# Kernel optimization log

Measured on AMD Instinct MI355X. Metric: run time of the kernel, lower is better.

Reference implementation:

```python
import jax, jax.numpy as jnp
import numpy as np

NUM_ITEMS = 100000
EMB_DIM = 146          # total output feature width
N_GENRES = 18          # fixed genre one-hot width
BATCH = 1048576


def setup_inputs() -> dict:
    key = jax.random.key(0)
    k1, k2, k3 = jax.random.split(key, 3)
    item_inputs = jax.random.randint(k1, (BATCH,), 0, NUM_ITEMS, dtype=jnp.int64)
    # learned embedding table, width = embedding_dim - 18
    item_embedding = jax.random.normal(k2, (NUM_ITEMS, EMB_DIM - N_GENRES), dtype=jnp.float32)
    # precomputed dense genre table: row i = one-hot genre vector for item i
    # (0/1 entries; items missing from the dict are all-zero rows)
    genre_table = (jax.random.uniform(k3, (NUM_ITEMS, N_GENRES)) < 0.15).astype(jnp.float32)
    return {"item_inputs": item_inputs, "item_embedding": item_embedding, "genre_table": genre_table}


def reference(item_inputs, item_embedding, genre_table):
    # fused double gather + concat: [B, 128] ++ [B, 18] -> [B, 146]
    item_embeds = item_embedding[item_inputs]   # embedding lookup
    item_genres = genre_table[item_inputs]      # vectorized replacement of python dict loop
    return jnp.concatenate([item_embeds, item_genres], axis=1)
```

## Files before the change

### kernel.cpp

```cpp
#include <hip/hip_runtime.h>


#define ROW_F2   73u
#define EMB_F2   64u
#define GENRE_F2 9u
#define TOTAL_F2 (1048576u * ROW_F2)

__global__ __launch_bounds__(256) void item_emb_gather_concat(
    const int* __restrict__ idx,
    const float2* __restrict__ emb,
    const float2* __restrict__ genre,
    float2* __restrict__ out)
{
    unsigned g = blockIdx.x * blockDim.x + threadIdx.x;
    if (g >= TOTAL_F2) return;

    unsigned row = g / ROW_F2;
    unsigned c2  = g - row * ROW_F2;

    int item = idx[row];

    float2 v;
    if (c2 < EMB_F2) {
        v = emb[(unsigned long long)item * EMB_F2 + c2];
    } else {
        v = genre[(unsigned long long)item * GENRE_F2 + (c2 - EMB_F2)];
    }
    out[g] = v;
}

extern "C" void kernel_launch(void* const* d_in, const int* in_sizes, int n_in,
                              void* d_out, int out_size, void* d_ws, size_t ws_size,
                              hipStream_t stream) {
    const int*    idx   = (const int*)d_in[0];
    const float2* emb   = (const float2*)d_in[1];
    const float2* genre = (const float2*)d_in[2];
    float2*       out   = (float2*)d_out;

    const unsigned block = 256;
    const unsigned grid  = (TOTAL_F2 + block - 1) / block;
    item_emb_gather_concat<<<grid, block, 0, stream>>>(idx, emb, genre, out);
}
```

Baseline: 785.6 us.

## Assign four rows per wavefront with vectorized index load and nontemporal stores

Replaces the one-thread-per-float2 mapping with one wavefront per four output rows. Each wave loads its four indices with a single int4 load, has each lane gather one float2 of each embedding row, and spreads the four genre slices across 36 lanes. Outputs are written with nontemporal stores. This removes the per-element division, repeated index loads and divergent branching, but relies on BATCH being a multiple of 16 and leaves some lanes idle during the genre gather.

Result: faster. 736.8 us (-6.2%).

```diff
diff --git a/kernel.cpp b/kernel.cpp
--- a/kernel.cpp
+++ b/kernel.cpp
@@ -1,43 +1,61 @@
 #include <hip/hip_runtime.h>
 
 
-#define ROW_F2   73u
-#define EMB_F2   64u
-#define GENRE_F2 9u
-#define TOTAL_F2 (1048576u * ROW_F2)
+#define BATCH     1048576u
+#define ROW_F2    73u
+#define EMB_F2    64u
+#define GENRE_F2  9u
+#define ROWS_PW   4u
+
+typedef float f32x2 __attribute__((ext_vector_type(2)));
 
 __global__ __launch_bounds__(256) void item_emb_gather_concat(
-    const int* __restrict__ idx,
-    const float2* __restrict__ emb,
-    const float2* __restrict__ genre,
-    float2* __restrict__ out)
+    const int*   __restrict__ idx,
+    const f32x2* __restrict__ emb,
+    const f32x2* __restrict__ genre,
+    f32x2*       __restrict__ out)
 {
-    unsigned g = blockIdx.x * blockDim.x + threadIdx.x;
-    if (g >= TOTAL_F2) return;
+    const unsigned lane = threadIdx.x & 63u;
 
-    unsigned row = g / ROW_F2;
-    unsigned c2  = g - row * ROW_F2;
+    unsigned wid_v = (blockIdx.x * 256u + threadIdx.x) >> 6;
+    const unsigned wid = (unsigned)__builtin_amdgcn_readfirstlane((int)wid_v);
+    const unsigned r0  = wid * ROWS_PW;
 
-    int item = idx[row];
+    const int4 it4 = *reinterpret_cast<const int4*>(idx + r0);
+    const unsigned i0 = (unsigned)it4.x;
+    const unsigned i1 = (unsigned)it4.y;
+    const unsigned i2 = (unsigned)it4.z;
+    const unsigned i3 = (unsigned)it4.w;
 
-    float2 v;
-    if (c2 < EMB_F2) {
-        v = emb[(unsigned long long)item * EMB_F2 + c2];
-    } else {
-        v = genre[(unsigned long long)item * GENRE_F2 + (c2 - EMB_F2)];
-    }
-    out[g] = v;
+    f32x2 e0 = emb[(size_t)i0 * EMB_F2 + lane];
+    f32x2 e1 = emb[(size_t)i1 * EMB_F2 + lane];
+    f32x2 e2 = emb[(size_t)i2 * EMB_F2 + lane];
+    f32x2 e3 = emb[(size_t)i3 * EMB_F2 + lane];
+
+    unsigned ri = lane / 9u;
+    unsigned c  = lane - ri * 9u;
+    unsigned item = ri < 2u ? (ri == 0u ? i0 : i1)
+                            : (ri == 2u ? i2 : i3);
+    f32x2 g = genre[(size_t)item * GENRE_F2 + c];
+
+    size_t ob = (size_t)r0 * ROW_F2;
+    __builtin_nontemporal_store(e0, &out[ob + 0u * ROW_F2 + lane]);
+    __builtin_nontemporal_store(e1, &out[ob + 1u * ROW_F2 + lane]);
+    __builtin_nontemporal_store(e2, &out[ob + 2u * ROW_F2 + lane]);
+    __builtin_nontemporal_store(e3, &out[ob + 3u * ROW_F2 + lane]);
+    if (lane < 36u)
+        __builtin_nontemporal_store(g, &out[ob + (size_t)ri * ROW_F2 + EMB_F2 + c]);
 }
 
 extern "C" void kernel_launch(void* const* d_in, const int* in_sizes, int n_in,
                               void* d_out, int out_size, void* d_ws, size_t ws_size,
                               hipStream_t stream) {
-    const int*    idx   = (const int*)d_in[0];
-    const float2* emb   = (const float2*)d_in[1];
-    const float2* genre = (const float2*)d_in[2];
-    float2*       out   = (float2*)d_out;
+    const int*   idx   = (const int*)d_in[0];
+    const f32x2* emb   = (const f32x2*)d_in[1];
+    const f32x2* genre = (const f32x2*)d_in[2];
+    f32x2*       out   = (f32x2*)d_out;
 
     const unsigned block = 256;
-    const unsigned grid  = (TOTAL_F2 + block - 1) / block;
+    const unsigned grid  = BATCH / 16u;
     item_emb_gather_concat<<<grid, block, 0, stream>>>(idx, emb, genre, out);
 }
```
